# Optimization experiments

Hardware: AMD Instinct MI355X
Metric: run time of the kernel (lower is better)

Reference implementation:

```python
import jax, jax.numpy as jnp
import numpy as np

B, V, E, H, L = 8, 200, 40000, 128, 3


def setup_inputs() -> dict:
    key = jax.random.key(0)
    ks = jax.random.split(key, 24)
    s = 1.0 / np.sqrt(H)
    inp = {
        "x": jax.random.normal(ks[0], (B, V, 2), jnp.float32),
        "e": jax.random.uniform(ks[1], (B, E), jnp.float32),
        "edge_index": jax.random.randint(ks[2], (B, 2, E), 0, V),
        # Embedder
        "node_W": jax.random.normal(ks[3], (2, H), jnp.float32) * 0.5,
        "node_b": jnp.zeros((H,), jnp.float32),
        "edge_W": jax.random.normal(ks[4], (1, H), jnp.float32) * 0.5,
        "edge_b": jnp.zeros((H,), jnp.float32),
        # GCN layers (stacked over L)
        "U_W": jax.random.normal(ks[5], (L, H, H), jnp.float32) * s,
        "U_b": jnp.zeros((L, H), jnp.float32),
        "V_W": jax.random.normal(ks[6], (L, H, H), jnp.float32) * s,
        "V_b": jnp.zeros((L, H), jnp.float32),
        "A_W": jax.random.normal(ks[7], (L, H, H), jnp.float32) * s,
        "A_b": jnp.zeros((L, H), jnp.float32),
        "B_W": jax.random.normal(ks[8], (L, H, H), jnp.float32) * s,
        "B_b": jnp.zeros((L, H), jnp.float32),
        "C_W": jax.random.normal(ks[9], (L, H, H), jnp.float32) * s,
        "C_b": jnp.zeros((L, H), jnp.float32),
        # Out MLP: hidden -> hidden -> 2
        "out_W1": jax.random.normal(ks[10], (H, H), jnp.float32) * s,
        "out_b1": jnp.zeros((H,), jnp.float32),
        "out_W2": jax.random.normal(ks[11], (H, 2), jnp.float32) * s,
        "out_b2": jnp.zeros((2,), jnp.float32),
    }
    return inp


def reference(x, e, edge_index, node_W, node_b, edge_W, edge_b,
              U_W, U_b, V_W, V_b, A_W, A_b, B_W, B_b, C_W, C_b,
              out_W1, out_b1, out_W2, out_b2):
    n_nodes = x.shape[1]
    n_layers = U_W.shape[0]

    def per_graph(xi, ei, idx):
        # Embedder: coords (V,2)->(V,H), distances (E,)->(E,H)
        xh = xi @ node_W + node_b
        eh = ei[:, None] @ edge_W + edge_b
        src, dst = idx[0], idx[1]
        for l in range(n_layers):
            gate = jax.nn.sigmoid(eh)                       # (E,H) edge gates
            vx = xh @ V_W[l] + V_b[l]                       # (V,H)
            agg = jax.ops.segment_sum(gate * vx[src], dst,
                                      num_segments=n_nodes)  # (V,H)
            x_new = xh + jax.nn.relu(xh @ U_W[l] + U_b[l] + agg)
            eh = eh + jax.nn.relu(eh @ A_W[l] + A_b[l]
                                  + (xh @ B_W[l] + B_b[l])[src]
                                  + (xh @ C_W[l] + C_b[l])[dst])
            xh = x_new
        h = jax.nn.relu(eh @ out_W1 + out_b1)
        return jax.nn.sigmoid(h @ out_W2 + out_b2)           # (E,2)

    # batch loop in the original torch code -> vmap here
    return jax.vmap(per_graph)(x, e, edge_index)
```

## Files before the change

### kernel.cpp

```cpp
#include <hip/hip_runtime.h>
#include <hip/hip_bf16.h>

#define NB 8
#define NV 200
#define NE 40000
#define NH 128
#define NL 3
#define EBLK 157

typedef __attribute__((ext_vector_type(8))) __bf16 bf16x8;
typedef __attribute__((ext_vector_type(8))) short s16x8;
typedef __attribute__((ext_vector_type(4))) float f32x4;

__device__ inline float sigmoidf_(float x){ return 1.0f/(1.0f + __expf(-x)); }

__device__ inline short f2b(float f){
  union{ float f; unsigned u; } v; v.f = f;
  unsigned u = v.u;
  u += 0x7fffu + ((u >> 16) & 1u);
  return (short)(u >> 16);
}
__device__ inline float b2f(short s){
  union{ unsigned u; float f; } v; v.u = ((unsigned)(unsigned short)s) << 16;
  return v.f;
}
__device__ inline void splitb(float x, short &hi, short &lo){
  hi = f2b(x);
  lo = f2b(x - b2f(hi));
}

__global__ __launch_bounds__(256) void k_embed_nodes(
    const float* __restrict__ x, const float* __restrict__ nW,
    const float* __restrict__ nb, float* __restrict__ xh)
{
  int i = blockIdx.x*256 + threadIdx.x;
  if (i >= NB*NV*NH) return;
  int h  = i & (NH-1);
  int bv = i >> 7;
  xh[i] = x[bv*2+0]*nW[h] + x[bv*2+1]*nW[NH+h] + nb[h];
}

__global__ __launch_bounds__(256) void k_trans_w(
    const float* __restrict__ AW, const float* __restrict__ oW1,
    short* __restrict__ Wt)
{
  int m = blockIdx.x;
  const float* src = (m < 3) ? (AW + m*NH*NH) : oW1;
  short* dhi = Wt + (size_t)m*NH*NH;
  short* dlo = Wt + (size_t)(4+m)*NH*NH;
  for (int i = threadIdx.x; i < NH*NH; i += 256){
    int n = i >> 7, c = i & 127;
    int k;
    if (m < 3){
      k = c;
    } else {
      int kk = c >> 5, lg = (c >> 3) & 3, jh = (c >> 2) & 1, jl = c & 3;
      k = 32*kk + 16*jh + 4*lg + jl;
    }
    short hi, lo;
    splitb(src[k*NH + n], hi, lo);
    dhi[i] = hi; dlo[i] = lo;
  }
}

__global__ __launch_bounds__(256) void k_zero(int* __restrict__ p, int n){
  int i = blockIdx.x*256 + threadIdx.x;
  if (i < n) p[i] = 0;
}

__global__ __launch_bounds__(256) void k_count(const int* __restrict__ ei, int* __restrict__ counts){
  int i = blockIdx.x*256 + threadIdx.x;
  if (i >= NB*NE) return;
  int b = i / NE, e = i % NE;
  int dv = ei[b*2*NE + NE + e];
  atomicAdd(&counts[b*NV + dv], 1);
}

__global__ void k_scan(const int* __restrict__ counts, int* __restrict__ offs, int* __restrict__ cursor){
  int b = blockIdx.x;
  if (threadIdx.x == 0){
    int run = 0;
    for (int v=0; v<NV; v++){
      offs[b*(NV+1)+v] = run;
      cursor[b*NV+v]   = run;
      run += counts[b*NV+v];
    }
    offs[b*(NV+1)+NV] = run;
  }
}

__global__ __launch_bounds__(256) void k_scatter(const int* __restrict__ ei, int* __restrict__ cursor, int* __restrict__ csr){
  int i = blockIdx.x*256 + threadIdx.x;
  if (i >= NB*NE) return;
  int b = i / NE, e = i % NE;
  int dv = ei[b*2*NE + NE + e];
  int pos = atomicAdd(&cursor[b*NV + dv], 1);
  csr[(size_t)b*NE + pos] = e;
}

__global__ __launch_bounds__(256) void k_node_mm(
    float* __restrict__ xh, const float* __restrict__ agg,
    const float* __restrict__ VWl, const float* __restrict__ Vbl,
    const float* __restrict__ BWl, const float* __restrict__ Bbl,
    const float* __restrict__ CWl, const float* __restrict__ Cbl,
    const float* __restrict__ UWl, const float* __restrict__ Ubl,
    float* __restrict__ vx, float* __restrict__ bx,
    float* __restrict__ cx, float* __restrict__ ux,
    int do_update)
{
  __shared__ float sx[NH];
  int b = blockIdx.x / NV, v = blockIdx.x % NV;
  size_t row = (size_t)b*NV + v;
  float* xr = xh + row*NH;
  int ht = threadIdx.x;
  if (ht < NH){
    float xv = xr[ht];
    if (do_update){
      float u = ux[row*NH + ht];
      #pragma unroll
      for (int p=0;p<4;p++) u += agg[(size_t)p*NB*NV*NH + row*NH + ht];
      xv += u > 0.f ? u : 0.f;
      xr[ht] = xv;
    }
    sx[ht] = xv;
  }
  __syncthreads();
  #pragma unroll
  for (int pass=0; pass<2; pass++){
    int t = threadIdx.x + pass*256;
    int mat = t >> 7, h = t & 127;
    const float* W = (mat==0) ? VWl : (mat==1) ? BWl : (mat==2) ? CWl : UWl;
    const float* bs = (mat==0) ? Vbl : (mat==1) ? Bbl : (mat==2) ? Cbl : Ubl;
    float* op = (mat==0) ? vx : (mat==1) ? bx : (mat==2) ? cx : ux;
    float acc = bs[h];
    #pragma unroll 8
    for (int k=0;k<NH;k++) acc += sx[k]*W[k*NH + h];
    op[row*NH + h] = acc;
  }
}

__global__ __launch_bounds__(128) void k_agg(
    const float* __restrict__ eh, const float* __restrict__ evec,
    const float* __restrict__ eWe, const float* __restrict__ ebe,
    const float* __restrict__ vx, const int* __restrict__ ei,
    const int* __restrict__ csr, const int* __restrict__ offs,
    float* __restrict__ agg, int is_l0)
{
  int part = blockIdx.x & 3;
  int bv   = blockIdx.x >> 2;
  int b = bv / NV, v = bv % NV;
  int h = threadIdx.x;
  const int* srcp  = ei + b*2*NE;
  const int* csrg  = csr + (size_t)b*NE;
  const float* ehg = eh + (size_t)b*NE*NH;
  const float* evg = evec + (size_t)b*NE;
  const float* vxg = vx + (size_t)b*NV*NH;
  float wh = eWe[h], bh = ebe[h];
  int beg = offs[b*(NV+1)+v], end = offs[b*(NV+1)+v+1];
  int len = end - beg;
  int i    = beg + ((len*part) >> 2);
  int stop = beg + ((len*(part+1)) >> 2);
  float acc = 0.f;
  for (; i+8 <= stop; i += 8){
    int   eb[8], sb[8];
    float a[8], w[8];
    #pragma unroll
    for (int j=0;j<8;j++) eb[j] = csrg[i+j];
    #pragma unroll
    for (int j=0;j<8;j++) sb[j] = srcp[eb[j]];
    if (is_l0){
      #pragma unroll
      for (int j=0;j<8;j++) a[j] = evg[eb[j]]*wh + bh;
    } else {
      #pragma unroll
      for (int j=0;j<8;j++) a[j] = ehg[(size_t)eb[j]*NH + h];
    }
    #pragma unroll
    for (int j=0;j<8;j++) w[j] = vxg[sb[j]*NH + h];
    #pragma unroll
    for (int j=0;j<8;j++) acc += sigmoidf_(a[j]) * w[j];
  }
  for (; i < stop; i++){
    int e0 = csrg[i]; int s0 = srcp[e0];
    float a = is_l0 ? (evg[e0]*wh + bh) : ehg[(size_t)e0*NH+h];
    acc += sigmoidf_(a) * vxg[s0*NH+h];
  }
  agg[((size_t)part*NB*NV + (size_t)b*NV + v)*NH + h] = acc;
}

__global__ __launch_bounds__(512) void k_edge_update(
    float* __restrict__ eh, const short* __restrict__ Wt,
    const float* __restrict__ Ab, const float* __restrict__ bx,
    const float* __restrict__ cx, const int* __restrict__ ei,
    const float* __restrict__ evec, const float* __restrict__ eWe,
    const float* __restrict__ ebe, int is_l0)
{
  __shared__ short sW[2*NH*NH];
  const short* Whi = Wt;
  const short* Wlo = Wt + 4*NH*NH;
  {
    #pragma unroll
    for (int i=0;i<8;i++){
      int sidx = (threadIdx.x + i*512)*8;
      int p = sidx >> 14, r = sidx & 16383;
      int hh = r >> 7, kw = r & 127;
      const short* src = p ? Wlo : Whi;
      s16x8 vv = *(const s16x8*)(src + r);
      *(s16x8*)(sW + p*16384 + hh*128 + (kw ^ ((hh&7)<<3))) = vv;
    }
  }
  __syncthreads();

  int blk  = blockIdx.x % EBLK;
  int b    = blockIdx.x / EBLK;
  int wave = threadIdx.x >> 6;
  int lane = threadIdx.x & 63;
  int l15 = lane & 15, lg = lane >> 4;
  int eA = blk*256 + wave*32 + l15;
  int eB = eA + 16;
  int eAc = eA < NE ? eA : NE-1;
  int eBc = eB < NE ? eB : NE-1;
  float* ehg = eh + (size_t)b*NE*NH;
  const int* srcp = ei + b*2*NE;
  int svA = srcp[eAc], dvA = srcp[NE+eAc];
  int svB = srcp[eBc], dvB = srcp[NE+eBc];

  float evA = 0.f, evB = 0.f;
  f32x4 rA[8], rB[8];
  if (is_l0){
    evA = evec[(size_t)b*NE + eAc];
    evB = evec[(size_t)b*NE + eBc];
    #pragma unroll
    for (int kk=0;kk<4;kk++){
      f32x4 w0 = *(const f32x4*)(eWe + kk*32 + lg*8);
      f32x4 w1 = *(const f32x4*)(eWe + kk*32 + lg*8 + 4);
      f32x4 q0 = *(const f32x4*)(ebe + kk*32 + lg*8);
      f32x4 q1 = *(const f32x4*)(ebe + kk*32 + lg*8 + 4);
      #pragma unroll
      for (int j=0;j<4;j++){
        rA[2*kk][j]   = evA*w0[j] + q0[j];
        rA[2*kk+1][j] = evA*w1[j] + q1[j];
        rB[2*kk][j]   = evB*w0[j] + q0[j];
        rB[2*kk+1][j] = evB*w1[j] + q1[j];
      }
    }
  } else {
    const float* pA = ehg + (size_t)eAc*NH + lg*8;
    const float* pB = ehg + (size_t)eBc*NH + lg*8;
    #pragma unroll
    for (int kk=0;kk<4;kk++){
      rA[2*kk]   = *(const f32x4*)(pA + kk*32);
      rA[2*kk+1] = *(const f32x4*)(pA + kk*32 + 4);
    }
    #pragma unroll
    for (int kk=0;kk<4;kk++){
      rB[2*kk]   = *(const f32x4*)(pB + kk*32);
      rB[2*kk+1] = *(const f32x4*)(pB + kk*32 + 4);
    }
  }

  bf16x8 ahA[4], alA[4], ahB[4], alB[4];
  #pragma unroll
  for (int kk=0;kk<4;kk++){
    union{ short s[8]; bf16x8 v; } uh, ul;
    #pragma unroll
    for (int j=0;j<4;j++){
      splitb(rA[2*kk][j],   uh.s[j],   ul.s[j]);
      splitb(rA[2*kk+1][j], uh.s[4+j], ul.s[4+j]);
    }
    ahA[kk] = uh.v; alA[kk] = ul.v;
  }
  #pragma unroll
  for (int kk=0;kk<4;kk++){
    union{ short s[8]; bf16x8 v; } uh, ul;
    #pragma unroll
    for (int j=0;j<4;j++){
      splitb(rB[2*kk][j],   uh.s[j],   ul.s[j]);
      splitb(rB[2*kk+1][j], uh.s[4+j], ul.s[4+j]);
    }
    ahB[kk] = uh.v; alB[kk] = ul.v;
  }

  f32x4 accA[8], accB[8];
  #pragma unroll
  for (int n=0;n<8;n++){ accA[n] = (f32x4){0.f,0.f,0.f,0.f}; accB[n] = (f32x4){0.f,0.f,0.f,0.f}; }

  #pragma unroll
  for (int kk=0;kk<4;kk++){
    #pragma unroll
    for (int n=0;n<8;n++){
      int row = n*16 + l15;
      int cofs = (kk*32 + lg*8) ^ ((l15&7)<<3);
      union{ s16x8 s; bf16x8 v; } wh, wl;
      wh.s = *(const s16x8*)(sW + row*128 + cofs);
      wl.s = *(const s16x8*)(sW + 16384 + row*128 + cofs);
      accA[n] = __builtin_amdgcn_mfma_f32_16x16x32_bf16(wh.v, ahA[kk], accA[n], 0, 0, 0);
      accA[n] = __builtin_amdgcn_mfma_f32_16x16x32_bf16(wh.v, alA[kk], accA[n], 0, 0, 0);
      accA[n] = __builtin_amdgcn_mfma_f32_16x16x32_bf16(wl.v, ahA[kk], accA[n], 0, 0, 0);
      accB[n] = __builtin_amdgcn_mfma_f32_16x16x32_bf16(wh.v, ahB[kk], accB[n], 0, 0, 0);
      accB[n] = __builtin_amdgcn_mfma_f32_16x16x32_bf16(wh.v, alB[kk], accB[n], 0, 0, 0);
      accB[n] = __builtin_amdgcn_mfma_f32_16x16x32_bf16(wl.v, ahB[kk], accB[n], 0, 0, 0);
    }
  }

  const float* bxA = bx + ((size_t)b*NV + svA)*NH;
  const float* cxA = cx + ((size_t)b*NV + dvA)*NH;
  const float* bxB = bx + ((size_t)b*NV + svB)*NH;
  const float* cxB = cx + ((size_t)b*NV + dvB)*NH;
  float* ehA = ehg + (size_t)eAc*NH;
  float* ehB = ehg + (size_t)eBc*NH;
  #pragma unroll
  for (int n=0;n<8;n++){
    int h0 = n*16 + lg*4;
    f32x4 ab4 = *(const f32x4*)(Ab + h0);
    f32x4 bA = *(const f32x4*)(bxA + h0);
    f32x4 cA = *(const f32x4*)(cxA + h0);
    f32x4 bB = *(const f32x4*)(bxB + h0);
    f32x4 cB = *(const f32x4*)(cxB + h0);
    f32x4 oA, oB;
    if (is_l0){
      f32x4 w4 = *(const f32x4*)(eWe + h0);
      f32x4 q4 = *(const f32x4*)(ebe + h0);
      #pragma unroll
      for (int j=0;j<4;j++){ oA[j] = evA*w4[j] + q4[j]; oB[j] = evB*w4[j] + q4[j]; }
    } else {
      oA = *(const f32x4*)(ehA + h0);
      oB = *(const f32x4*)(ehB + h0);
    }
    f32x4 nA, nB;
    #pragma unroll
    for (int j=0;j<4;j++){
      float vA = accA[n][j] + ab4[j] + bA[j] + cA[j];
      vA = vA > 0.f ? vA : 0.f;
      nA[j] = oA[j] + vA;
      float vB = accB[n][j] + ab4[j] + bB[j] + cB[j];
      vB = vB > 0.f ? vB : 0.f;
      nB[j] = oB[j] + vB;
    }
    if (eA < NE) *(f32x4*)(ehA + h0) = nA;
    if (eB < NE) *(f32x4*)(ehB + h0) = nB;
  }
}

__global__ __launch_bounds__(512) void k_edge_out(
    const float* __restrict__ eh, const short* __restrict__ Wt,
    const float* __restrict__ Ab, const float* __restrict__ bx,
    const float* __restrict__ cx, const int* __restrict__ ei,
    const float* __restrict__ b1, const float* __restrict__ W2,
    const float* __restrict__ b2, float* __restrict__ out)
{
  __shared__ short sW[4*NH*NH];
  {
    const short* A2hi = Wt + 2*NH*NH;
    const short* A2lo = Wt + 6*NH*NH;
    const short* W1hi = Wt + 3*NH*NH;
    const short* W1lo = Wt + 7*NH*NH;
    #pragma unroll
    for (int i=0;i<16;i++){
      int sidx = (threadIdx.x + i*512)*8;
      int p = i >> 2;
      int r = sidx & 16383;
      int hh = r >> 7, kw = r & 127;
      const short* src = (p==0)? A2hi : (p==1)? A2lo : (p==2)? W1hi : W1lo;
      s16x8 vv = *(const s16x8*)(src + r);
      *(s16x8*)(sW + p*16384 + hh*128 + (kw ^ ((hh&7)<<3))) = vv;
    }
  }
  __syncthreads();

  int blk  = blockIdx.x % EBLK;
  int b    = blockIdx.x / EBLK;
  int wave = threadIdx.x >> 6;
  int lane = threadIdx.x & 63;
  int l15 = lane & 15, lg = lane >> 4;
  int eA = blk*256 + wave*32 + l15;
  int eB = eA + 16;
  int eAc = eA < NE ? eA : NE-1;
  int eBc = eB < NE ? eB : NE-1;
  const float* ehg = eh + (size_t)b*NE*NH;
  const int* srcp = ei + b*2*NE;
  int svA = srcp[eAc], dvA = srcp[NE+eAc];
  int svB = srcp[eBc], dvB = srcp[NE+eBc];

  const float* pA = ehg + (size_t)eAc*NH + lg*8;
  const float* pB = ehg + (size_t)eBc*NH + lg*8;
  f32x4 rA[8], rB[8];
  #pragma unroll
  for (int kk=0;kk<4;kk++){
    rA[2*kk]   = *(const f32x4*)(pA + kk*32);
    rA[2*kk+1] = *(const f32x4*)(pA + kk*32 + 4);
  }
  #pragma unroll
  for (int kk=0;kk<4;kk++){
    rB[2*kk]   = *(const f32x4*)(pB + kk*32);
    rB[2*kk+1] = *(const f32x4*)(pB + kk*32 + 4);
  }

  bf16x8 ahA[4], alA[4], ahB[4], alB[4];
  #pragma unroll
  for (int kk=0;kk<4;kk++){
    union{ short s[8]; bf16x8 v; } uh, ul;
    #pragma unroll
    for (int j=0;j<4;j++){
      splitb(rA[2*kk][j],   uh.s[j],   ul.s[j]);
      splitb(rA[2*kk+1][j], uh.s[4+j], ul.s[4+j]);
    }
    ahA[kk] = uh.v; alA[kk] = ul.v;
  }
  #pragma unroll
  for (int kk=0;kk<4;kk++){
    union{ short s[8]; bf16x8 v; } uh, ul;
    #pragma unroll
    for (int j=0;j<4;j++){
      splitb(rB[2*kk][j],   uh.s[j],   ul.s[j]);
      splitb(rB[2*kk+1][j], uh.s[4+j], ul.s[4+j]);
    }
    ahB[kk] = uh.v; alB[kk] = ul.v;
  }

  f32x4 accA[8], accB[8];
  #pragma unroll
  for (int n=0;n<8;n++){ accA[n] = (f32x4){0.f,0.f,0.f,0.f}; accB[n] = (f32x4){0.f,0.f,0.f,0.f}; }
  #pragma unroll
  for (int kk=0;kk<4;kk++){
    #pragma unroll
    for (int n=0;n<8;n++){
      int row = n*16 + l15;
      int cofs = (kk*32 + lg*8) ^ ((l15&7)<<3);
      union{ s16x8 s; bf16x8 v; } wh, wl;
      wh.s = *(const s16x8*)(sW + row*128 + cofs);
      wl.s = *(const s16x8*)(sW + 16384 + row*128 + cofs);
      accA[n] = __builtin_amdgcn_mfma_f32_16x16x32_bf16(wh.v, ahA[kk], accA[n], 0, 0, 0);
      accA[n] = __builtin_amdgcn_mfma_f32_16x16x32_bf16(wh.v, alA[kk], accA[n], 0, 0, 0);
      accA[n] = __builtin_amdgcn_mfma_f32_16x16x32_bf16(wl.v, ahA[kk], accA[n], 0, 0, 0);
      accB[n] = __builtin_amdgcn_mfma_f32_16x16x32_bf16(wh.v, ahB[kk], accB[n], 0, 0, 0);
      accB[n] = __builtin_amdgcn_mfma_f32_16x16x32_bf16(wh.v, alB[kk], accB[n], 0, 0, 0);
      accB[n] = __builtin_amdgcn_mfma_f32_16x16x32_bf16(wl.v, ahB[kk], accB[n], 0, 0, 0);
    }
  }

  const float* bxA = bx + ((size_t)b*NV + svA)*NH;
  const float* cxA = cx + ((size_t)b*NV + dvA)*NH;
  const float* bxB = bx + ((size_t)b*NV + svB)*NH;
  const float* cxB = cx + ((size_t)b*NV + dvB)*NH;
  const float* ehA = ehg + (size_t)eAc*NH;
  const float* ehB = ehg + (size_t)eBc*NH;
  bf16x8 qhA[4], qlA[4], qhB[4], qlB[4];
  #pragma unroll
  for (int kk=0;kk<4;kk++){
    union{ short s[8]; bf16x8 v; } uhA, ulA, uhB, ulB;
    #pragma unroll
    for (int half=0; half<2; half++){
      int n = 2*kk + half;
      int h0 = n*16 + lg*4;
      f32x4 ab4 = *(const f32x4*)(Ab + h0);
      f32x4 bA4 = *(const f32x4*)(bxA + h0);
      f32x4 cA4 = *(const f32x4*)(cxA + h0);
      f32x4 oA4 = *(const f32x4*)(ehA + h0);
      f32x4 bB4 = *(const f32x4*)(bxB + h0);
      f32x4 cB4 = *(const f32x4*)(cxB + h0);
      f32x4 oB4 = *(const f32x4*)(ehB + h0);
      #pragma unroll
      for (int j=0;j<4;j++){
        float vA = accA[n][j] + ab4[j] + bA4[j] + cA4[j];
        vA = vA > 0.f ? vA : 0.f;
        float e3A = oA4[j] + vA;
        splitb(e3A, uhA.s[half*4+j], ulA.s[half*4+j]);
        float vB = accB[n][j] + ab4[j] + bB4[j] + cB4[j];
        vB = vB > 0.f ? vB : 0.f;
        float e3B = oB4[j] + vB;
        splitb(e3B, uhB.s[half*4+j], ulB.s[half*4+j]);
      }
    }
    qhA[kk] = uhA.v; qlA[kk] = ulA.v;
    qhB[kk] = uhB.v; qlB[kk] = ulB.v;
  }

  f32x4 acc2A[8], acc2B[8];
  #pragma unroll
  for (int n=0;n<8;n++){ acc2A[n] = (f32x4){0.f,0.f,0.f,0.f}; acc2B[n] = (f32x4){0.f,0.f,0.f,0.f}; }
  #pragma unroll
  for (int kk=0;kk<4;kk++){
    #pragma unroll
    for (int n=0;n<8;n++){
      int row = n*16 + l15;
      int cofs = (kk*32 + lg*8) ^ ((l15&7)<<3);
      union{ s16x8 s; bf16x8 v; } wh, wl;
      wh.s = *(const s16x8*)(sW + 2*16384 + row*128 + cofs);
      wl.s = *(const s16x8*)(sW + 3*16384 + row*128 + cofs);
      acc2A[n] = __builtin_amdgcn_mfma_f32_16x16x32_bf16(wh.v, qhA[kk], acc2A[n], 0, 0, 0);
      acc2A[n] = __builtin_amdgcn_mfma_f32_16x16x32_bf16(wh.v, qlA[kk], acc2A[n], 0, 0, 0);
      acc2A[n] = __builtin_amdgcn_mfma_f32_16x16x32_bf16(wl.v, qhA[kk], acc2A[n], 0, 0, 0);
      acc2B[n] = __builtin_amdgcn_mfma_f32_16x16x32_bf16(wh.v, qhB[kk], acc2B[n], 0, 0, 0);
      acc2B[n] = __builtin_amdgcn_mfma_f32_16x16x32_bf16(wh.v, qlB[kk], acc2B[n], 0, 0, 0);
      acc2B[n] = __builtin_amdgcn_mfma_f32_16x16x32_bf16(wl.v, qhB[kk], acc2B[n], 0, 0, 0);
    }
  }

  float p0A = 0.f, p1A = 0.f, p0B = 0.f, p1B = 0.f;
  #pragma unroll
  for (int n=0;n<8;n++){
    int h0 = n*16 + lg*4;
    f32x4 b14 = *(const f32x4*)(b1 + h0);
    f32x4 wA  = *(const f32x4*)(W2 + h0*2);
    f32x4 wB  = *(const f32x4*)(W2 + h0*2 + 4);
    #pragma unroll
    for (int j=0;j<4;j++){
      float w20 = (j<2) ? wA[2*j]   : wB[2*(j-2)];
      float w21 = (j<2) ? wA[2*j+1] : wB[2*(j-2)+1];
      float hA = acc2A[n][j] + b14[j]; hA = hA > 0.f ? hA : 0.f;
      float hB = acc2B[n][j] + b14[j]; hB = hB > 0.f ? hB : 0.f;
      p0A += hA*w20; p1A += hA*w21;
      p0B += hB*w20; p1B += hB*w21;
    }
  }
  p0A += __shfl_xor(p0A, 16, 64); p0A += __shfl_xor(p0A, 32, 64);
  p1A += __shfl_xor(p1A, 16, 64); p1A += __shfl_xor(p1A, 32, 64);
  p0B += __shfl_xor(p0B, 16, 64); p0B += __shfl_xor(p0B, 32, 64);
  p1B += __shfl_xor(p1B, 16, 64); p1B += __shfl_xor(p1B, 32, 64);
  if (lg == 0){
    float bb0 = b2[0], bb1 = b2[1];
    if (eA < NE){
      float2 r; r.x = sigmoidf_(p0A + bb0); r.y = sigmoidf_(p1A + bb1);
      *(float2*)(out + ((size_t)b*NE + eA)*2) = r;
    }
    if (eB < NE){
      float2 r; r.x = sigmoidf_(p0B + bb0); r.y = sigmoidf_(p1B + bb1);
      *(float2*)(out + ((size_t)b*NE + eB)*2) = r;
    }
  }
}

extern "C" void kernel_launch(void* const* d_in, const int* in_sizes, int n_in,
                              void* d_out, int out_size, void* d_ws, size_t ws_size,
                              hipStream_t stream)
{
  const float* x   = (const float*)d_in[0];
  const float* e   = (const float*)d_in[1];
  const int*   ei  = (const int*)d_in[2];
  const float* nW  = (const float*)d_in[3];
  const float* nb  = (const float*)d_in[4];
  const float* eW  = (const float*)d_in[5];
  const float* eb  = (const float*)d_in[6];
  const float* UW  = (const float*)d_in[7];
  const float* Ub  = (const float*)d_in[8];
  const float* VW  = (const float*)d_in[9];
  const float* Vb  = (const float*)d_in[10];
  const float* AW  = (const float*)d_in[11];
  const float* Ab  = (const float*)d_in[12];
  const float* BW  = (const float*)d_in[13];
  const float* Bb  = (const float*)d_in[14];
  const float* CW  = (const float*)d_in[15];
  const float* Cb  = (const float*)d_in[16];
  const float* oW1 = (const float*)d_in[17];
  const float* ob1 = (const float*)d_in[18];
  const float* oW2 = (const float*)d_in[19];
  const float* ob2 = (const float*)d_in[20];
  float* out = (float*)d_out;

  char* ws = (char*)d_ws;
  size_t off = 0;
  auto alloc = [&](size_t bytes)->char*{
    char* p = ws + off;
    off += (bytes + 255) & ~(size_t)255;
    return p;
  };
  float* eh     = (float*)alloc((size_t)NB*NE*NH*4);
  float* xh     = (float*)alloc((size_t)NB*NV*NH*4);
  float* vx     = (float*)alloc((size_t)NB*NV*NH*4);
  float* bx     = (float*)alloc((size_t)NB*NV*NH*4);
  float* cx     = (float*)alloc((size_t)NB*NV*NH*4);
  float* ux     = (float*)alloc((size_t)NB*NV*NH*4);
  float* agg    = (float*)alloc((size_t)4*NB*NV*NH*4);
  short* Wt     = (short*)alloc((size_t)8*NH*NH*2);
  int* counts   = (int*)alloc((size_t)NB*NV*4);
  int* cursor   = (int*)alloc((size_t)NB*NV*4);
  int* offs     = (int*)alloc((size_t)NB*(NV+1)*4);
  int* csr      = (int*)alloc((size_t)NB*NE*4);
  (void)ws_size; (void)in_sizes; (void)n_in; (void)out_size;

  k_embed_nodes<<<(NB*NV*NH+255)/256, 256, 0, stream>>>(x, nW, nb, xh);
  k_trans_w<<<4, 256, 0, stream>>>(AW, oW1, Wt);
  k_zero<<<(NB*NV+255)/256, 256, 0, stream>>>(counts, NB*NV);
  k_count<<<(NB*NE+255)/256, 256, 0, stream>>>(ei, counts);
  k_scan<<<NB, 64, 0, stream>>>(counts, offs, cursor);
  k_scatter<<<(NB*NE+255)/256, 256, 0, stream>>>(ei, cursor, csr);

  for (int l=0; l<NL; l++){
    k_node_mm<<<NB*NV, 256, 0, stream>>>(xh, agg,
        VW + l*NH*NH, Vb + l*NH, BW + l*NH*NH, Bb + l*NH,
        CW + l*NH*NH, Cb + l*NH, UW + l*NH*NH, Ub + l*NH,
        vx, bx, cx, ux, l > 0 ? 1 : 0);
    if (l < NL-1)
      k_agg<<<NB*NV*4, 128, 0, stream>>>(eh, e, eW, eb, vx, ei, csr, offs, agg, l==0 ? 1 : 0);
    if (l < NL-1)
      k_edge_update<<<NB*EBLK, 512, 0, stream>>>(eh, Wt + l*NH*NH, Ab + l*NH, bx, cx, ei,
                                                 e, eW, eb, l==0 ? 1 : 0);
    else
      k_edge_out<<<NB*EBLK, 512, 0, stream>>>(eh, Wt, Ab + l*NH, bx, cx, ei,
                                              ob1, oW2, ob2, out);
  }
}
```

Measured before the change: 532.0 us.

## Replace CSR gather aggregation with edge-order shared-memory atomic scatter

Removes the CSR build (count, scan, scatter kernels) and the per-node gather aggregation. Each block now handles a contiguous chunk of edges for one graph, reads eh rows coalesced in edge order, and accumulates gate*vx into a 100KB shared-memory node buffer with atomics. The buffer is then flushed to global memory with atomics into a pre-zeroed agg array. This trades the CSR setup and random eh row gathers for shared and global atomics, shared-memory pressure that lowers occupancy, and float summation order that depends on scheduling.

```diff
diff --git a/kernel.cpp b/kernel.cpp
--- a/kernel.cpp
+++ b/kernel.cpp
@@ -7,6 +7,7 @@
 #define NH 128
 #define NL 3
 #define EBLK 157
+#define NPART 32
 
 typedef __attribute__((ext_vector_type(8))) __bf16 bf16x8;
 typedef __attribute__((ext_vector_type(8))) short s16x8;
@@ -63,39 +64,9 @@
   }
 }
 
-__global__ __launch_bounds__(256) void k_zero(int* __restrict__ p, int n){
+__global__ __launch_bounds__(256) void k_zero_f(float* __restrict__ p, int n4){
   int i = blockIdx.x*256 + threadIdx.x;
-  if (i < n) p[i] = 0;
-}
-
-__global__ __launch_bounds__(256) void k_count(const int* __restrict__ ei, int* __restrict__ counts){
-  int i = blockIdx.x*256 + threadIdx.x;
-  if (i >= NB*NE) return;
-  int b = i / NE, e = i % NE;
-  int dv = ei[b*2*NE + NE + e];
-  atomicAdd(&counts[b*NV + dv], 1);
-}
-
-__global__ void k_scan(const int* __restrict__ counts, int* __restrict__ offs, int* __restrict__ cursor){
-  int b = blockIdx.x;
-  if (threadIdx.x == 0){
-    int run = 0;
-    for (int v=0; v<NV; v++){
-      offs[b*(NV+1)+v] = run;
-      cursor[b*NV+v]   = run;
-      run += counts[b*NV+v];
-    }
-    offs[b*(NV+1)+NV] = run;
-  }
-}
-
-__global__ __launch_bounds__(256) void k_scatter(const int* __restrict__ ei, int* __restrict__ cursor, int* __restrict__ csr){
-  int i = blockIdx.x*256 + threadIdx.x;
-  if (i >= NB*NE) return;
-  int b = i / NE, e = i % NE;
-  int dv = ei[b*2*NE + NE + e];
-  int pos = atomicAdd(&cursor[b*NV + dv], 1);
-  csr[(size_t)b*NE + pos] = e;
+  if (i < n4) *(f32x4*)(p + i*4) = (f32x4){0.f,0.f,0.f,0.f};
 }
 
 __global__ __launch_bounds__(256) void k_node_mm(
@@ -116,9 +87,7 @@
   if (ht < NH){
     float xv = xr[ht];
     if (do_update){
-      float u = ux[row*NH + ht];
-      #pragma unroll
-      for (int p=0;p<4;p++) u += agg[(size_t)p*NB*NV*NH + row*NH + ht];
+      float u = ux[row*NH + ht] + agg[row*NH + ht];
       xv += u > 0.f ? u : 0.f;
       xr[ht] = xv;
     }
@@ -139,53 +108,59 @@
   }
 }
 
-__global__ __launch_bounds__(128) void k_agg(
+__global__ __launch_bounds__(512) void k_agg2(
     const float* __restrict__ eh, const float* __restrict__ evec,
     const float* __restrict__ eWe, const float* __restrict__ ebe,
     const float* __restrict__ vx, const int* __restrict__ ei,
-    const int* __restrict__ csr, const int* __restrict__ offs,
     float* __restrict__ agg, int is_l0)
 {
-  int part = blockIdx.x & 3;
-  int bv   = blockIdx.x >> 2;
-  int b = bv / NV, v = bv % NV;
-  int h = threadIdx.x;
-  const int* srcp  = ei + b*2*NE;
-  const int* csrg  = csr + (size_t)b*NE;
+  __shared__ float s_agg[NV*NH];
+  for (int i = threadIdx.x; i < NV*NH; i += 512) s_agg[i] = 0.f;
+  __syncthreads();
+
+  int part = blockIdx.x % NPART;
+  int b    = blockIdx.x / NPART;
+  int h    = threadIdx.x & 127;
+  int sub  = threadIdx.x >> 7;
+  const int* srcp = ei + b*2*NE;
+  const int* dstp = srcp + NE;
   const float* ehg = eh + (size_t)b*NE*NH;
   const float* evg = evec + (size_t)b*NE;
   const float* vxg = vx + (size_t)b*NV*NH;
   float wh = eWe[h], bh = ebe[h];
-  int beg = offs[b*(NV+1)+v], end = offs[b*(NV+1)+v+1];
-  int len = end - beg;
-  int i    = beg + ((len*part) >> 2);
-  int stop = beg + ((len*(part+1)) >> 2);
-  float acc = 0.f;
-  for (; i+8 <= stop; i += 8){
-    int   eb[8], sb[8];
-    float a[8], w[8];
-    #pragma unroll
-    for (int j=0;j<8;j++) eb[j] = csrg[i+j];
-    #pragma unroll
-    for (int j=0;j<8;j++) sb[j] = srcp[eb[j]];
+  int e0 = part*(NE/NPART);
+  int e1 = e0 + NE/NPART;
+
+  int e = e0 + sub;
+  for (; e + 12 < e1; e += 16){
+    int sv[4], dv[4];
+    float a[4], w[4];
+    #pragma unroll
+    for (int j=0;j<4;j++){ sv[j] = srcp[e + 4*j]; dv[j] = dstp[e + 4*j]; }
     if (is_l0){
       #pragma unroll
-      for (int j=0;j<8;j++) a[j] = evg[eb[j]]*wh + bh;
+      for (int j=0;j<4;j++) a[j] = evg[e + 4*j]*wh + bh;
     } else {
       #pragma unroll
-      for (int j=0;j<8;j++) a[j] = ehg[(size_t)eb[j]*NH + h];
-    }
-    #pragma unroll
-    for (int j=0;j<8;j++) w[j] = vxg[sb[j]*NH + h];
-    #pragma unroll
-    for (int j=0;j<8;j++) acc += sigmoidf_(a[j]) * w[j];
-  }
-  for (; i < stop; i++){
-    int e0 = csrg[i]; int s0 = srcp[e0];
-    float a = is_l0 ? (evg[e0]*wh + bh) : ehg[(size_t)e0*NH+h];
-    acc += sigmoidf_(a) * vxg[s0*NH+h];
-  }
-  agg[((size_t)part*NB*NV + (size_t)b*NV + v)*NH + h] = acc;
+      for (int j=0;j<4;j++) a[j] = ehg[(size_t)(e + 4*j)*NH + h];
+    }
+    #pragma unroll
+    for (int j=0;j<4;j++) w[j] = vxg[sv[j]*NH + h];
+    #pragma unroll
+    for (int j=0;j<4;j++) atomicAdd(&s_agg[dv[j]*NH + h], sigmoidf_(a[j])*w[j]);
+  }
+  for (; e < e1; e += 4){
+    int sv = srcp[e], dv = dstp[e];
+    float a = is_l0 ? (evg[e]*wh + bh) : ehg[(size_t)e*NH + h];
+    atomicAdd(&s_agg[dv*NH + h], sigmoidf_(a)*vxg[sv*NH + h]);
+  }
+
+  __syncthreads();
+  float* aggg = agg + (size_t)b*NV*NH;
+  for (int i = threadIdx.x; i < NV*NH; i += 512){
+    float v = s_agg[i];
+    if (v != 0.f) atomicAdd(&aggg[i], v);
+  }
 }
 
 __global__ __launch_bounds__(512) void k_edge_update(
@@ -571,28 +546,22 @@
   float* bx     = (float*)alloc((size_t)NB*NV*NH*4);
   float* cx     = (float*)alloc((size_t)NB*NV*NH*4);
   float* ux     = (float*)alloc((size_t)NB*NV*NH*4);
-  float* agg    = (float*)alloc((size_t)4*NB*NV*NH*4);
+  float* agg    = (float*)alloc((size_t)NB*NV*NH*4);
   short* Wt     = (short*)alloc((size_t)8*NH*NH*2);
-  int* counts   = (int*)alloc((size_t)NB*NV*4);
-  int* cursor   = (int*)alloc((size_t)NB*NV*4);
-  int* offs     = (int*)alloc((size_t)NB*(NV+1)*4);
-  int* csr      = (int*)alloc((size_t)NB*NE*4);
   (void)ws_size; (void)in_sizes; (void)n_in; (void)out_size;
 
   k_embed_nodes<<<(NB*NV*NH+255)/256, 256, 0, stream>>>(x, nW, nb, xh);
   k_trans_w<<<4, 256, 0, stream>>>(AW, oW1, Wt);
-  k_zero<<<(NB*NV+255)/256, 256, 0, stream>>>(counts, NB*NV);
-  k_count<<<(NB*NE+255)/256, 256, 0, stream>>>(ei, counts);
-  k_scan<<<NB, 64, 0, stream>>>(counts, offs, cursor);
-  k_scatter<<<(NB*NE+255)/256, 256, 0, stream>>>(ei, cursor, csr);
 
   for (int l=0; l<NL; l++){
     k_node_mm<<<NB*NV, 256, 0, stream>>>(xh, agg,
         VW + l*NH*NH, Vb + l*NH, BW + l*NH*NH, Bb + l*NH,
         CW + l*NH*NH, Cb + l*NH, UW + l*NH*NH, Ub + l*NH,
         vx, bx, cx, ux, l > 0 ? 1 : 0);
-    if (l < NL-1)
-      k_agg<<<NB*NV*4, 128, 0, stream>>>(eh, e, eW, eb, vx, ei, csr, offs, agg, l==0 ? 1 : 0);
+    if (l < NL-1){
+      k_zero_f<<<(NB*NV*NH/4+255)/256, 256, 0, stream>>>(agg, NB*NV*NH/4);
+      k_agg2<<<NB*NPART, 512, 0, stream>>>(eh, e, eW, eb, vx, ei, agg, l==0 ? 1 : 0);
+    }
     if (l < NL-1)
       k_edge_update<<<NB*EBLK, 512, 0, stream>>>(eh, Wt + l*NH*NH, Ab + l*NH, bx, cx, ei,
                                                  e, eW, eb, l==0 ? 1 : 0);
```

Measured after the change: 828.9 us. 55.8% more time.
